# Optimization experiments

Hardware: AMD Instinct MI355X
Metric: run time of the kernel (lower is better)

The kernel has to match this reference:

```python
import jax, jax.numpy as jnp
import numpy as np

N, E, G, D, L = 200000, 400000, 1024, 300, 5
BN_EPS = 1e-5


def setup_inputs() -> dict:
    key = jax.random.key(0)
    ks = jax.random.split(key, 14)
    s = 0.1  # param init scale
    return {
        "atomic_number": jax.random.randint(ks[0], (N,), 0, 120),
        "chirality_type": jax.random.randint(ks[1], (N,), 0, 3),
        "bond_type": jax.random.randint(ks[2], (E,), 0, 6),
        "bond_direction_type": jax.random.randint(ks[3], (E,), 0, 3),
        "src": jax.random.randint(ks[4], (E,), 0, N),
        "dst": jax.random.randint(ks[5], (E,), 0, N),
        "graph_ids": jnp.sort(jax.random.randint(ks[6], (N,), 0, G)),
        "num_graphs": G,
        "node_emb0": jax.random.normal(ks[7], (120, D), jnp.float32) * s,
        "node_emb1": jax.random.normal(ks[8], (3, D), jnp.float32) * s,
        "edge_emb0": jax.random.normal(ks[9], (L, 6, D), jnp.float32) * s,
        "edge_emb1": jax.random.normal(ks[10], (L, 3, D), jnp.float32) * s,
        "W1": jax.random.normal(ks[11], (L, D, 2 * D), jnp.float32) * (1.0 / np.sqrt(D)),
        "b1": jnp.zeros((L, 2 * D), jnp.float32),
        "W2": jax.random.normal(ks[12], (L, 2 * D, D), jnp.float32) * (1.0 / np.sqrt(2 * D)),
        "b2": jnp.zeros((L, D), jnp.float32),
        "bn_gamma": jnp.ones((L, D), jnp.float32),
        "bn_beta": jnp.zeros((L, D), jnp.float32),
        "bn_mean": jnp.zeros((L, D), jnp.float32),
        "bn_var": jnp.ones((L, D), jnp.float32),
        "Wd": jax.random.normal(ks[13], (D, 256), jnp.float32) * (1.0 / np.sqrt(D)),
        "bd": jnp.zeros((256,), jnp.float32),
    }


def reference(atomic_number, chirality_type, bond_type, bond_direction_type,
              src, dst, graph_ids, num_graphs,
              node_emb0, node_emb1, edge_emb0, edge_emb1,
              W1, b1, W2, b2, bn_gamma, bn_beta, bn_mean, bn_var, Wd, bd):
    n = atomic_number.shape[0]
    # input node embedding: sum of the two categorical lookups
    h = node_emb0[atomic_number] + node_emb1[chirality_type]  # [N, D]
    for l in range(L):
        # per-layer edge embedding (sum of bond-type / bond-direction lookups)
        e = edge_emb0[l][bond_type] + edge_emb1[l][bond_direction_type]  # [E, D]
        # message u_add_e, sum reduce onto destination nodes
        m = h[src] + e
        agg = jax.ops.segment_sum(m, dst, num_segments=n)  # [N, D]
        # GIN MLP: Linear(D,2D) -> ReLU -> Linear(2D,D)
        h = jax.nn.relu(agg @ W1[l] + b1[l]) @ W2[l] + b2[l]
        # BatchNorm1d in eval mode (running stats)
        h = (h - bn_mean[l]) * jax.lax.rsqrt(bn_var[l] + BN_EPS) * bn_gamma[l] + bn_beta[l]
        if l < L - 1:  # ReLU on all but last layer (dropout is identity in eval)
            h = jax.nn.relu(h)
    # AvgPooling over nodes of each graph
    gsum = jax.ops.segment_sum(h, graph_ids, num_segments=num_graphs)  # [G, D]
    cnt = jax.ops.segment_sum(jnp.ones((n, 1), h.dtype), graph_ids, num_segments=num_graphs)
    gavg = gsum / jnp.maximum(cnt, 1.0)
    # head: Dropout (eval identity) + Linear(300, 256), then squeeze (no-op here)
    return jnp.squeeze(gavg @ Wd + bd)
```

## Files before the change

kernel.cpp:

```cpp
#include <hip/hip_runtime.h>
#include <hip/hip_bf16.h>
#include <hip/hip_fp16.h>

#define D 300
#define D2 150
#define HD 600
#define NLAYERS 5
#define BN_EPS 1e-5f

#define KS1 10
#define NT1 5
#define KS2 20
#define NT2 3
#define P1 (NT1*KS1*4096)
#define P2 (NT2*KS2*4096)

#define SCAN_BLK 1024

typedef _Float16 f16x8 __attribute__((ext_vector_type(8)));
typedef __attribute__((ext_vector_type(4))) float f32x4;

__device__ inline ushort f2h(float x) {
    __half h = __float2half(x);
    return *reinterpret_cast<ushort*>(&h);
}
__device__ inline float h2f(ushort u) {
    __half h;
    *reinterpret_cast<ushort*>(&h) = u;
    return __half2float(h);
}
__device__ inline uint pack2h(float lo, float hi) {
    return (uint)f2h(lo) | ((uint)f2h(hi) << 16);
}

__global__ __launch_bounds__(256) void zero_kernel(uint4* __restrict__ p, long n4)
{
    long i = (long)blockIdx.x * blockDim.x + threadIdx.x;
    long stride = (long)gridDim.x * blockDim.x;
    uint4 z = make_uint4(0u, 0u, 0u, 0u);
    for (; i < n4; i += stride) p[i] = z;
}

__global__ __launch_bounds__(256) void embed_kernel(
    const int* __restrict__ an, const int* __restrict__ ch,
    const float* __restrict__ e0, const float* __restrict__ e1,
    uint* __restrict__ h_u, int N)
{
    int node = blockIdx.x * 4 + (threadIdx.x >> 6);
    if (node >= N) return;
    int lane = threadIdx.x & 63;
    const float* r0 = e0 + (size_t)an[node] * D;
    const float* r1 = e1 + (size_t)ch[node] * D;
    uint* hr = h_u + (size_t)node * D2;
    for (int d2 = lane; d2 < D2; d2 += 64) {
        float2 a = *(const float2*)(r0 + d2 * 2);
        float2 b = *(const float2*)(r1 + d2 * 2);
        hr[d2] = pack2h(a.x + b.x, a.y + b.y);
    }
}

__global__ __launch_bounds__(256) void count_kernel(
    const int* __restrict__ dst, int* __restrict__ deg, int E)
{
    int e = blockIdx.x * 256 + threadIdx.x;
    if (e < E) atomicAdd(&deg[dst[e]], 1);
}

__global__ __launch_bounds__(256) void scan_part_kernel(
    const int* __restrict__ deg, int* __restrict__ part, int N)
{
    __shared__ int sm[256];
    int b = blockIdx.x, t = threadIdx.x;
    int base = b * SCAN_BLK + t * 4;
    int s = 0;
#pragma unroll
    for (int j = 0; j < 4; ++j) { int i = base + j; if (i < N) s += deg[i]; }
    sm[t] = s;
    __syncthreads();
    for (int off = 128; off > 0; off >>= 1) {
        if (t < off) sm[t] += sm[t + off];
        __syncthreads();
    }
    if (t == 0) part[b] = sm[0];
}

__global__ __launch_bounds__(256) void scan_top_kernel(int* __restrict__ part, int NB)
{
    __shared__ int sm[256];
    int t = threadIdx.x;
    int own = (t < NB) ? part[t] : 0;
    sm[t] = own;
    __syncthreads();
    for (int off = 1; off < 256; off <<= 1) {
        int u = (t >= off) ? sm[t - off] : 0;
        __syncthreads();
        sm[t] += u;
        __syncthreads();
    }
    if (t < NB) part[t] = sm[t] - own;
}

__global__ __launch_bounds__(256) void scan_write_kernel(
    const int* __restrict__ deg, const int* __restrict__ part,
    int* __restrict__ offsets, int* __restrict__ cursor, int N, int E)
{
    __shared__ int sm[256];
    int b = blockIdx.x, t = threadIdx.x;
    int base = b * SCAN_BLK + t * 4;
    int v[4], s = 0;
#pragma unroll
    for (int j = 0; j < 4; ++j) { int i = base + j; v[j] = (i < N) ? deg[i] : 0; s += v[j]; }
    int own = s;
    sm[t] = s;
    __syncthreads();
    for (int off = 1; off < 256; off <<= 1) {
        int u = (t >= off) ? sm[t - off] : 0;
        __syncthreads();
        sm[t] += u;
        __syncthreads();
    }
    int ex = sm[t] - own + part[b];
#pragma unroll
    for (int j = 0; j < 4; ++j) {
        int i = base + j;
        if (i < N) { offsets[i] = ex; cursor[i] = ex; ex += v[j]; }
    }
    if (b == 0 && t == 0) offsets[N] = E;
}

__global__ __launch_bounds__(256) void scatter_kernel(
    const int* __restrict__ dst, int* __restrict__ cursor,
    int* __restrict__ csr, int E)
{
    int e = blockIdx.x * 256 + threadIdx.x;
    if (e < E) {
        int pos = atomicAdd(&cursor[dst[e]], 1);
        csr[pos] = e;
    }
}

__global__ __launch_bounds__(256) void eprep_kernel(
    const int* __restrict__ csr, const int* __restrict__ src,
    const int* __restrict__ bt, const int* __restrict__ bd,
    int* __restrict__ esrc, unsigned char* __restrict__ ecomb, int E)
{
    int p = blockIdx.x * 256 + threadIdx.x;
    if (p < E) {
        int e = csr[p];
        esrc[p] = src[e];
        ecomb[p] = (unsigned char)(bt[e] * 3 + bd[e]);
    }
}

__global__ __launch_bounds__(256) void etab_kernel(
    const float* __restrict__ ee0, const float* __restrict__ ee1,
    uint* __restrict__ etab)
{
    int i = blockIdx.x * 256 + threadIdx.x;
    const int total = NLAYERS * 18 * D2;
    if (i >= total) return;
    int d2 = i % D2;
    int rest = i / D2;
    int c = rest % 18, l = rest / 18;
    int btv = c / 3, bdv = c % 3;
    const float* r0 = ee0 + ((size_t)l * 6 + btv) * D + d2 * 2;
    const float* r1 = ee1 + ((size_t)l * 3 + bdv) * D + d2 * 2;
    etab[i] = pack2h(r0[0] + r1[0], r0[1] + r1[1]);
}

__global__ void prep_bn_kernel(
    const float* __restrict__ b2, const float* __restrict__ gamma,
    const float* __restrict__ beta, const float* __restrict__ mean,
    const float* __restrict__ var, float* __restrict__ scale2,
    float* __restrict__ shift2, int n)
{
    int i = blockIdx.x * blockDim.x + threadIdx.x;
    if (i >= n) return;
    float s = gamma[i] * rsqrtf(var[i] + BN_EPS);
    scale2[i] = s;
    shift2[i] = (b2[i] - mean[i]) * s + beta[i];
}

__global__ __launch_bounds__(256) void conv_w_kernel(
    const float* __restrict__ W1, const float* __restrict__ W2,
    ushort* __restrict__ w1h, ushort* __restrict__ w2h)
{
    int i = blockIdx.x * blockDim.x + threadIdx.x;
    const int PER = P1 + P2;
    if (i >= NLAYERS * PER) return;
    int l = i / PER;
    int r = i - l * PER;
    float v;
    ushort* ph;
    if (r < P1) {
        int pos = r;
        int j = pos & 7, c = (pos >> 3) & 127, kg = (pos >> 10) & 3;
        int rest = pos >> 12;
        int ks = rest % KS1, nt = rest / KS1;
        int k = ks * 32 + kg * 8 + j, n = nt * 128 + c;
        v = (k < D && n < HD) ? W1[(size_t)l * D * HD + (size_t)k * HD + n] : 0.f;
        ph = w1h + (size_t)l * P1 + pos;
    } else {
        int pos = r - P1;
        int j = pos & 7, c = (pos >> 3) & 127, kg = (pos >> 10) & 3;
        int rest = pos >> 12;
        int ks = rest % KS2, nt = rest / KS2;
        int k = ks * 32 + kg * 8 + j, n = nt * 128 + c;
        v = (k < HD && n < D) ? W2[(size_t)l * HD * D + (size_t)k * D + n] : 0.f;
        ph = w2h + (size_t)l * P2 + pos;
    }
    *ph = f2h(v);
}

template<bool RELU2>
__global__ __launch_bounds__(512, 4) void fused_mlp_kernel(
    const uint* __restrict__ Hin,
    const uint* __restrict__ etab_l,
    const int* __restrict__ esrc, const unsigned char* __restrict__ ecomb,
    const int* __restrict__ offsets,
    const uint4* __restrict__ B1,
    const uint4* __restrict__ B2,
    const float* __restrict__ bias1,
    const float* __restrict__ scale2,
    const float* __restrict__ shift2,
    uint* __restrict__ Hout,
    int M)
{
    __shared__ ushort lds[KS2 * 4 * 64 * 8];

    int t = threadIdx.x;
    int lane = t & 63;
    int wid = t >> 6;
    int lanelo = lane & 15;
    int kg = lane >> 4;
    int m0 = blockIdx.x * 64;

    {
        uint* ldsAu = (uint*)lds;
        int rbase = wid * 8;
        for (int rr = 0; rr < 8; ++rr) {
            int rowl = rbase + rr;
            int v = m0 + rowl;
            float ax0 = 0.f, ay0 = 0.f, ax1 = 0.f, ay1 = 0.f, ax2 = 0.f, ay2 = 0.f;
            if (v < M) {
                int p0 = offsets[v], p1 = offsets[v + 1];
                for (int p = p0; p < p1; ++p) {
                    int s = esrc[p];
                    int c = ecomb[p];
                    const uint* hr = Hin + (size_t)s * D2;
                    const uint* er = etab_l + c * D2;
                    int d0 = lane, d1 = lane + 64, dq = lane + 128;
                    uint hv0 = hr[d0], ev0 = er[d0];
                    uint hv1 = hr[d1], ev1 = er[d1];
                    uint hv2 = 0u, ev2 = 0u;
                    if (dq < D2) { hv2 = hr[dq]; ev2 = er[dq]; }
                    ax0 += h2f((ushort)(hv0 & 0xffffu)) + h2f((ushort)(ev0 & 0xffffu));
                    ay0 += h2f((ushort)(hv0 >> 16))     + h2f((ushort)(ev0 >> 16));
                    ax1 += h2f((ushort)(hv1 & 0xffffu)) + h2f((ushort)(ev1 & 0xffffu));
                    ay1 += h2f((ushort)(hv1 >> 16))     + h2f((ushort)(ev1 >> 16));
                    ax2 += h2f((ushort)(hv2 & 0xffffu)) + h2f((ushort)(ev2 & 0xffffu));
                    ay2 += h2f((ushort)(hv2 >> 16))     + h2f((ushort)(ev2 >> 16));
                }
            }
            {
                int d2 = lane;
                int q = d2 >> 2;
                ldsAu[(q * 64 + (rowl ^ (q & 7))) * 4 + (d2 & 3)] = pack2h(ax0, ay0);
                d2 = lane + 64;
                q = d2 >> 2;
                ldsAu[(q * 64 + (rowl ^ (q & 7))) * 4 + (d2 & 3)] = pack2h(ax1, ay1);
                d2 = lane + 128;
                if (d2 < 160) {
                    uint val = (d2 < D2) ? pack2h(ax2, ay2) : 0u;
                    q = d2 >> 2;
                    ldsAu[(q * 64 + (rowl ^ (q & 7))) * 4 + (d2 & 3)] = val;
                }
            }
        }
    }
    __syncthreads();

    {
        f32x4 acc[4][5];
#pragma unroll
        for (int mi = 0; mi < 4; ++mi)
#pragma unroll
            for (int ni = 0; ni < 5; ++ni) {
                f32x4 z = {0.f, 0.f, 0.f, 0.f};
                acc[mi][ni] = z;
            }

        int addrb[5];
#pragma unroll
        for (int ni = 0; ni < 5; ++ni) {
            int col = wid * 80 + ni * 16 + lanelo;
            int nt = col >> 7, c = col & 127;
            addrb[ni] = nt * (KS1 * 512) + kg * 128 + c;
        }

        uint4 bn[5];
#pragma unroll
        for (int ni = 0; ni < 5; ++ni) bn[ni] = B1[addrb[ni]];

        const f16x8* ap = (const f16x8*)lds;
#pragma unroll
        for (int ks = 0; ks < KS1; ++ks) {
            uint4 bc[5];
#pragma unroll
            for (int ni = 0; ni < 5; ++ni) bc[ni] = bn[ni];
            if (ks + 1 < KS1) {
#pragma unroll
                for (int ni = 0; ni < 5; ++ni) bn[ni] = B1[addrb[ni] + (ks + 1) * 512];
            }
            int q1 = ks * 4 + kg;
            int ab = q1 * 64 + (lanelo ^ (q1 & 7));
            f16x8 a0 = ap[ab];
            f16x8 a1 = ap[ab + 16];
            f16x8 a2 = ap[ab + 32];
            f16x8 a3 = ap[ab + 48];
#pragma unroll
            for (int ni = 0; ni < 5; ++ni) {
                f16x8 b = *(const f16x8*)&bc[ni];
                acc[0][ni] = __builtin_amdgcn_mfma_f32_16x16x32_f16(a0, b, acc[0][ni], 0, 0, 0);
                acc[1][ni] = __builtin_amdgcn_mfma_f32_16x16x32_f16(a1, b, acc[1][ni], 0, 0, 0);
                acc[2][ni] = __builtin_amdgcn_mfma_f32_16x16x32_f16(a2, b, acc[2][ni], 0, 0, 0);
                acc[3][ni] = __builtin_amdgcn_mfma_f32_16x16x32_f16(a3, b, acc[3][ni], 0, 0, 0);
            }
        }

        __syncthreads();

        uint* ldsHu = (uint*)lds;
#pragma unroll
        for (int ni = 0; ni < 5; ++ni) {
            int col = wid * 80 + ni * 16 + lanelo;
            float bias = (col < HD) ? bias1[col] : 0.f;
            int ks2 = col >> 5, g2 = (col >> 3) & 3, j2 = col & 7;
            int dbase = (ks2 * 4 + g2) * 256 + (j2 >> 1);
#pragma unroll
            for (int mi = 0; mi < 4; ++mi) {
                int r0 = mi * 16 + kg * 4;
#pragma unroll
                for (int r = 0; r < 4; ++r) {
                    float y = fmaxf(acc[mi][ni][r] + bias, 0.f);
                    float yn = __shfl_xor(y, 1);
                    if ((lanelo & 1) == 0)
                        ldsHu[dbase + (r0 + r) * 4] = pack2h(y, yn);
                }
            }
        }
    }
    __syncthreads();

    {
        f32x4 acc[4][3];
#pragma unroll
        for (int mi = 0; mi < 4; ++mi)
#pragma unroll
            for (int ni = 0; ni < 3; ++ni) {
                f32x4 z = {0.f, 0.f, 0.f, 0.f};
                acc[mi][ni] = z;
            }

        int addrb[3];
#pragma unroll
        for (int ni = 0; ni < 3; ++ni) {
            int col = wid * 48 + ni * 16 + lanelo;
            int nt = col >> 7, c = col & 127;
            addrb[ni] = nt * (KS2 * 512) + kg * 128 + c;
        }

        uint4 bn[3];
#pragma unroll
        for (int ni = 0; ni < 3; ++ni) bn[ni] = B2[addrb[ni]];

        const f16x8* hp = (const f16x8*)lds;
#pragma unroll
        for (int ks = 0; ks < KS2; ++ks) {
            uint4 bc[3];
#pragma unroll
            for (int ni = 0; ni < 3; ++ni) bc[ni] = bn[ni];
            if (ks + 1 < KS2) {
#pragma unroll
                for (int ni = 0; ni < 3; ++ni) bn[ni] = B2[addrb[ni] + (ks + 1) * 512];
            }
            int ab = (ks * 4 + kg) * 64 + lanelo;
            f16x8 a0 = hp[ab];
            f16x8 a1 = hp[ab + 16];
            f16x8 a2 = hp[ab + 32];
            f16x8 a3 = hp[ab + 48];
#pragma unroll
            for (int ni = 0; ni < 3; ++ni) {
                f16x8 b = *(const f16x8*)&bc[ni];
                acc[0][ni] = __builtin_amdgcn_mfma_f32_16x16x32_f16(a0, b, acc[0][ni], 0, 0, 0);
                acc[1][ni] = __builtin_amdgcn_mfma_f32_16x16x32_f16(a1, b, acc[1][ni], 0, 0, 0);
                acc[2][ni] = __builtin_amdgcn_mfma_f32_16x16x32_f16(a2, b, acc[2][ni], 0, 0, 0);
                acc[3][ni] = __builtin_amdgcn_mfma_f32_16x16x32_f16(a3, b, acc[3][ni], 0, 0, 0);
            }
        }

        __syncthreads();

        uint* stg = (uint*)lds;
#pragma unroll
        for (int ni = 0; ni < 3; ++ni) {
            int col = wid * 48 + ni * 16 + lanelo;
            float sc = 1.f, sh = 0.f;
            if (col < D) { sc = scale2[col]; sh = shift2[col]; }
#pragma unroll
            for (int mi = 0; mi < 4; ++mi) {
                int r0 = mi * 16 + kg * 4;
#pragma unroll
                for (int r = 0; r < 4; ++r) {
                    float y = acc[mi][ni][r] * sc + sh;
                    if (RELU2) y = fmaxf(y, 0.f);
                    float yn = __shfl_xor(y, 1);
                    if ((lanelo & 1) == 0 && col < D)
                        stg[(r0 + r) * 154 + (col >> 1)] = pack2h(y, yn);
                }
            }
        }
    }
    __syncthreads();

    {
        const uint* stg = (const uint*)lds;
#pragma unroll
        for (int i = 0; i < 19; ++i) {
            int g = t + i * 512;
            if (g < 64 * 150) {
                int row = g / 150, c = g - row * 150;
                if (m0 + row < M)
                    Hout[(size_t)(m0 + row) * D2 + c] = stg[row * 154 + c];
            }
        }
    }
}

__global__ __launch_bounds__(320) void pool_kernel(
    const ushort* __restrict__ h, const int* __restrict__ gid,
    float* __restrict__ gavg, int N)
{
    int g = blockIdx.x;
    int lo = 0, hi = N;
    while (lo < hi) { int mid = (lo + hi) >> 1; if (gid[mid] < g) lo = mid + 1; else hi = mid; }
    int start = lo;
    lo = start; hi = N;
    while (lo < hi) { int mid = (lo + hi) >> 1; if (gid[mid] <= g) lo = mid + 1; else hi = mid; }
    int end = lo;
    int d = threadIdx.x;
    if (d >= D) return;
    float s = 0.f;
    for (int i = start; i < end; ++i) s += h2f(h[(size_t)i * D + d]);
    float cnt = (float)(end - start);
    gavg[(size_t)g * D + d] = s / fmaxf(cnt, 1.f);
}

__global__ __launch_bounds__(256) void head_kernel(
    const float* __restrict__ gavg, const float* __restrict__ Wd,
    const float* __restrict__ bd, float* __restrict__ out)
{
    int g = blockIdx.x;
    int j = threadIdx.x;
    float s = bd[j];
    const float* gr = gavg + (size_t)g * D;
    for (int d = 0; d < D; ++d) s = fmaf(gr[d], Wd[(size_t)d * 256 + j], s);
    out[(size_t)g * 256 + j] = s;
}

extern "C" void kernel_launch(void* const* d_in, const int* in_sizes, int n_in,
                              void* d_out, int out_size, void* d_ws, size_t ws_size,
                              hipStream_t stream)
{
    const int*   atomic_number = (const int*)d_in[0];
    const int*   chirality     = (const int*)d_in[1];
    const int*   bond_type     = (const int*)d_in[2];
    const int*   bond_dir      = (const int*)d_in[3];
    const int*   src           = (const int*)d_in[4];
    const int*   dst           = (const int*)d_in[5];
    const int*   graph_ids     = (const int*)d_in[6];
    const float* node_emb0     = (const float*)d_in[8];
    const float* node_emb1     = (const float*)d_in[9];
    const float* edge_emb0     = (const float*)d_in[10];
    const float* edge_emb1     = (const float*)d_in[11];
    const float* W1            = (const float*)d_in[12];
    const float* b1            = (const float*)d_in[13];
    const float* W2            = (const float*)d_in[14];
    const float* b2            = (const float*)d_in[15];
    const float* bn_gamma      = (const float*)d_in[16];
    const float* bn_beta       = (const float*)d_in[17];
    const float* bn_mean       = (const float*)d_in[18];
    const float* bn_var        = (const float*)d_in[19];
    const float* Wd            = (const float*)d_in[20];
    const float* bd            = (const float*)d_in[21];

    int N = in_sizes[0];
    int E = in_sizes[2];
    int G = out_size / 256;
    float* out = (float*)d_out;

    char* ws = (char*)d_ws;
    size_t offs = 0;
    auto take = [&](size_t nbytes) -> char* {
        char* p = ws + offs;
        offs += (nbytes + 255) & ~(size_t)255;
        return p;
    };
    ushort* w1h    = (ushort*)take((size_t)NLAYERS * P1 * 2);
    ushort* w2h    = (ushort*)take((size_t)NLAYERS * P2 * 2);
    uint*   h0     = (uint*)take((size_t)N * D2 * 4);
    uint*   h1     = (uint*)take((size_t)N * D2 * 4);
    int*    deg    = (int*)take((size_t)N * 4);
    int*    offsets= (int*)take((size_t)(N + 1) * 4);
    int*    cursor = (int*)take((size_t)N * 4);
    int*    csr    = (int*)take((size_t)E * 4);
    int*    esrc   = (int*)take((size_t)E * 4);
    unsigned char* ecomb = (unsigned char*)take((size_t)E);
    uint*   etab   = (uint*)take((size_t)NLAYERS * 18 * D2 * 4);
    int*    part   = (int*)take((size_t)256 * 4);
    float*  gavg   = (float*)take((size_t)G * D * 4);
    float*  scale2 = (float*)take((size_t)NLAYERS * D * 4);
    float*  shift2 = (float*)take((size_t)NLAYERS * D * 4);

    prep_bn_kernel<<<(NLAYERS * D + 255) / 256, 256, 0, stream>>>(
        b2, bn_gamma, bn_beta, bn_mean, bn_var, scale2, shift2, NLAYERS * D);
    {
        int T = NLAYERS * (P1 + P2);
        conv_w_kernel<<<(T + 255) / 256, 256, 0, stream>>>(W1, W2, w1h, w2h);
    }
    etab_kernel<<<(NLAYERS * 18 * D2 + 255) / 256, 256, 0, stream>>>(
        edge_emb0, edge_emb1, etab);
    embed_kernel<<<(N + 3) / 4, 256, 0, stream>>>(
        atomic_number, chirality, node_emb0, node_emb1, h0, N);

    int NB = (N + SCAN_BLK - 1) / SCAN_BLK;
    zero_kernel<<<(int)(((size_t)N + 1023) / 1024), 256, 0, stream>>>((uint4*)deg, (long)N / 4);
    count_kernel<<<(E + 255) / 256, 256, 0, stream>>>(dst, deg, E);
    scan_part_kernel<<<NB, 256, 0, stream>>>(deg, part, N);
    scan_top_kernel<<<1, 256, 0, stream>>>(part, NB);
    scan_write_kernel<<<NB, 256, 0, stream>>>(deg, part, offsets, cursor, N, E);
    scatter_kernel<<<(E + 255) / 256, 256, 0, stream>>>(dst, cursor, csr, E);
    eprep_kernel<<<(E + 255) / 256, 256, 0, stream>>>(csr, src, bond_type, bond_dir, esrc, ecomb, E);

    int mlp_grid = (N + 63) / 64;
    for (int l = 0; l < NLAYERS; ++l) {
        const uint* hin = (l & 1) ? h1 : h0;
        uint* hout      = (l & 1) ? h0 : h1;
        if (l < NLAYERS - 1)
            fused_mlp_kernel<true><<<mlp_grid, 512, 0, stream>>>(
                hin, etab + (size_t)l * 18 * D2, esrc, ecomb, offsets,
                (const uint4*)(w1h + (size_t)l * P1),
                (const uint4*)(w2h + (size_t)l * P2),
                b1 + (size_t)l * HD,
                scale2 + (size_t)l * D, shift2 + (size_t)l * D,
                hout, N);
        else
            fused_mlp_kernel<false><<<mlp_grid, 512, 0, stream>>>(
                hin, etab + (size_t)l * 18 * D2, esrc, ecomb, offsets,
                (const uint4*)(w1h + (size_t)l * P1),
                (const uint4*)(w2h + (size_t)l * P2),
                b1 + (size_t)l * HD,
                scale2 + (size_t)l * D, shift2 + (size_t)l * D,
                hout, N);
    }

    pool_kernel<<<G, 320, 0, stream>>>((const ushort*)h1, graph_ids, gavg, N);
    head_kernel<<<G, 256, 0, stream>>>(gavg, Wd, bd, out);
}
```

Measured before the change: 1.841 ms.

## Gather four rows per wave in aggregation and double-prefetch W2 tiles

The edge aggregation now has each wave work on four destination rows at once, with 16 lanes per row and each lane holding ten feature pairs. Before, a whole wave handled one row at a time over eight sequential rows. This gives more independent gather streams in flight to hide latency, but lanes will diverge because rows have different edge counts, and register use rises. The second GEMM also prefetches B2 fragments two k-steps ahead instead of one, which adds registers and one redundant load at the tail.

After: 1.680 ms (median of 3 runs). -8.7%, faster.

```diff
diff --git a/kernel.cpp b/kernel.cpp
--- a/kernel.cpp
+++ b/kernel.cpp
@@ -237,11 +237,15 @@
 
     {
         uint* ldsAu = (uint*)lds;
-        int rbase = wid * 8;
-        for (int rr = 0; rr < 8; ++rr) {
-            int rowl = rbase + rr;
+        int q = lane >> 4;
+        int ql = lane & 15;
+#pragma unroll
+        for (int pass = 0; pass < 2; ++pass) {
+            int rowl = wid * 8 + pass * 4 + q;
             int v = m0 + rowl;
-            float ax0 = 0.f, ay0 = 0.f, ax1 = 0.f, ay1 = 0.f, ax2 = 0.f, ay2 = 0.f;
+            float ax[10], ay[10];
+#pragma unroll
+            for (int j = 0; j < 10; ++j) { ax[j] = 0.f; ay[j] = 0.f; }
             if (v < M) {
                 int p0 = offsets[v], p1 = offsets[v + 1];
                 for (int p = p0; p < p1; ++p) {
@@ -249,32 +253,23 @@
                     int c = ecomb[p];
                     const uint* hr = Hin + (size_t)s * D2;
                     const uint* er = etab_l + c * D2;
-                    int d0 = lane, d1 = lane + 64, dq = lane + 128;
-                    uint hv0 = hr[d0], ev0 = er[d0];
-                    uint hv1 = hr[d1], ev1 = er[d1];
-                    uint hv2 = 0u, ev2 = 0u;
-                    if (dq < D2) { hv2 = hr[dq]; ev2 = er[dq]; }
-                    ax0 += h2f((ushort)(hv0 & 0xffffu)) + h2f((ushort)(ev0 & 0xffffu));
-                    ay0 += h2f((ushort)(hv0 >> 16))     + h2f((ushort)(ev0 >> 16));
-                    ax1 += h2f((ushort)(hv1 & 0xffffu)) + h2f((ushort)(ev1 & 0xffffu));
-                    ay1 += h2f((ushort)(hv1 >> 16))     + h2f((ushort)(ev1 >> 16));
-                    ax2 += h2f((ushort)(hv2 & 0xffffu)) + h2f((ushort)(ev2 & 0xffffu));
-                    ay2 += h2f((ushort)(hv2 >> 16))     + h2f((ushort)(ev2 >> 16));
+#pragma unroll
+                    for (int j = 0; j < 10; ++j) {
+                        int d2 = ql + j * 16;
+                        if (d2 < D2) {
+                            uint hv = hr[d2];
+                            uint ev = er[d2];
+                            ax[j] += h2f((ushort)(hv & 0xffffu)) + h2f((ushort)(ev & 0xffffu));
+                            ay[j] += h2f((ushort)(hv >> 16))     + h2f((ushort)(ev >> 16));
+                        }
+                    }
                 }
             }
-            {
-                int d2 = lane;
-                int q = d2 >> 2;
-                ldsAu[(q * 64 + (rowl ^ (q & 7))) * 4 + (d2 & 3)] = pack2h(ax0, ay0);
-                d2 = lane + 64;
-                q = d2 >> 2;
-                ldsAu[(q * 64 + (rowl ^ (q & 7))) * 4 + (d2 & 3)] = pack2h(ax1, ay1);
-                d2 = lane + 128;
-                if (d2 < 160) {
-                    uint val = (d2 < D2) ? pack2h(ax2, ay2) : 0u;
-                    q = d2 >> 2;
-                    ldsAu[(q * 64 + (rowl ^ (q & 7))) * 4 + (d2 & 3)] = val;
-                }
+#pragma unroll
+            for (int j = 0; j < 10; ++j) {
+                int d2 = ql + j * 16;
+                int qc = d2 >> 2;
+                ldsAu[(qc * 64 + (rowl ^ (qc & 7))) * 4 + (d2 & 3)] = pack2h(ax[j], ay[j]);
             }
         }
     }
@@ -370,19 +365,24 @@
             addrb[ni] = nt * (KS2 * 512) + kg * 128 + c;
         }
 
-        uint4 bn[3];
-#pragma unroll
-        for (int ni = 0; ni < 3; ++ni) bn[ni] = B2[addrb[ni]];
+        uint4 bn0[3], bn1[3];
+#pragma unroll
+        for (int ni = 0; ni < 3; ++ni) bn0[ni] = B2[addrb[ni]];
+#pragma unroll
+        for (int ni = 0; ni < 3; ++ni) bn1[ni] = B2[addrb[ni] + 512];
 
         const f16x8* hp = (const f16x8*)lds;
 #pragma unroll
         for (int ks = 0; ks < KS2; ++ks) {
             uint4 bc[3];
 #pragma unroll
-            for (int ni = 0; ni < 3; ++ni) bc[ni] = bn[ni];
-            if (ks + 1 < KS2) {
-#pragma unroll
-                for (int ni = 0; ni < 3; ++ni) bn[ni] = B2[addrb[ni] + (ks + 1) * 512];
+            for (int ni = 0; ni < 3; ++ni) bc[ni] = bn0[ni];
+#pragma unroll
+            for (int ni = 0; ni < 3; ++ni) bn0[ni] = bn1[ni];
+            {
+                int nk = (ks + 2 < KS2) ? ks + 2 : KS2 - 1;
+#pragma unroll
+                for (int ni = 0; ni < 3; ++ni) bn1[ni] = B2[addrb[ni] + nk * 512];
             }
             int ab = (ks * 4 + kg) * 64 + lanelo;
             f16x8 a0 = hp[ab];
```
